# Optimization experiments

Hardware: AMD Instinct MI355X
Metric: run time of the kernel (lower is better)

The kernel has to match this reference:

```python
import jax, jax.numpy as jnp
import numpy as np
from jax import lax

N_NODES = 8192
N_FEAT = 256
N_EDGES = 131072


def _cc_labels(src, dst, n):
    """Weakly-connected-component labels via min-label propagation + pointer jumping.
    Converged label[i] == min node index in i's component (matches scipy's
    first-occurrence labeling order after compaction)."""
    def cond(state):
        return state[1]

    def body(state):
        label, _ = state
        m = jnp.minimum(label[src], label[dst])
        new = label.at[src].min(m).at[dst].min(m)
        new = new[new]  # pointer jump
        return new, jnp.any(new != label)

    label, _ = lax.while_loop(cond, body, (jnp.arange(n, dtype=jnp.int32), jnp.array(True)))
    return label


def setup_inputs() -> dict:
    key = jax.random.key(0)
    k1, k2, k3 = jax.random.split(key, 3)
    x = jax.random.normal(k1, (N_NODES, N_FEAT), dtype=jnp.float32)
    edge_index = jax.random.randint(k2, (2, N_EDGES), 0, N_NODES, dtype=jnp.int32)
    batch = jnp.zeros((N_NODES,), dtype=jnp.int32)
    lin_w = jax.random.normal(k3, (1, 2 * N_FEAT), dtype=jnp.float32) * 0.05
    lin_b = jnp.zeros((1,), dtype=jnp.float32)
    return {"x": x, "edge_index": edge_index, "batch": batch, "lin_w": lin_w, "lin_b": lin_b}


def reference(x, edge_index, batch, lin_w, lin_b):
    n, f = x.shape
    src, dst = edge_index[0], edge_index[1]
    msk = src != dst  # drop self loops (kept in buffer, zeroed via mask for static shapes)
    # undirected: add flipped edges -> 2E directed edges
    src2 = jnp.concatenate([src, dst])
    dst2 = jnp.concatenate([dst, src])
    m2 = jnp.concatenate([msk, msk])
    mf = m2.astype(x.dtype)

    # edge score: Linear(2F,1) on [x[src] || x[dst]] == x@w1 gathered + x@w2 gathered
    w1, w2 = lin_w[0, :f], lin_w[0, f:]
    p1 = x @ w1  # [N]
    p2 = x @ w2  # [N]
    e = jnp.tanh(p1[src2] + p2[dst2] + lin_b[0])  # [2E]

    # contracted edges: score > threshold (0.0); masked edges excluded
    contract = m2 & (e > 0.0)
    srcc = jnp.where(contract, src2, 0)
    dstc = jnp.where(contract, dst2, 0)
    label = _cc_labels(srcc, dstc, n)
    # compact labels in order of smallest node index per component (== scipy ordering)
    is_root = (label == jnp.arange(n, dtype=label.dtype))
    cluster = (jnp.cumsum(is_root.astype(jnp.int32)) - 1)[label]  # [N], values in [0, K)

    # dense adjacency A and score adjacency S (scatter-add, like to_dense_adj)
    A = jnp.zeros((n, n), x.dtype).at[src2, dst2].add(mf)
    S = jnp.zeros((n, n), x.dtype).at[src2, dst2].add(e * mf)

    # isolated nodes w.r.t. contracted adjacency -> S[i,i] = 1
    cint = contract.astype(jnp.int32)
    deg = jnp.zeros(n, jnp.int32).at[src2].add(cint) + jnp.zeros(n, jnp.int32).at[dst2].add(cint)
    isolated = deg == 0
    idx = jnp.arange(n)
    S = S.at[idx, idx].set(jnp.where(isolated, jnp.ones((), x.dtype), S[idx, idx]))

    # X_new = (S @ C).T @ X = C.T @ (S.T @ X)  -- C.T@ is a segment-sum over clusters
    # (padded to N rows; rows >= num_clusters are zero)
    X_new = jax.ops.segment_sum(S.T @ x, cluster, num_segments=n)

    # coarsened adjacency C.T @ A @ C with zero diagonal (dense, padded to NxN)
    M1 = jax.ops.segment_sum(A, cluster, num_segments=n)        # pool rows
    A_c = jax.ops.segment_sum(M1.T, cluster, num_segments=n).T  # pool cols
    A_c = A_c.at[idx, idx].set(0.0)

    new_batch = jnp.zeros(n, batch.dtype).at[cluster].set(batch)
    return X_new, A_c, new_batch, cluster
```

## Files before the change

kernel.cpp:

```cpp
#include <hip/hip_runtime.h>
#include <math.h>

#define N_NODES 8192
#define N_FEAT  256
#define N_EDGES 131072
#define N_DIR   (2*N_EDGES)


__device__ __forceinline__ void edge_sd(const int* __restrict__ ei, int k, int& s, int& d){
  s = ei[k];
  d = (k < N_EDGES) ? ei[k + N_EDGES] : ei[k - N_EDGES];
}

__device__ __forceinline__ int rep_lds(int v, int* L){
  int curr = L[v];
  if (curr != v){
    int prev = v, next;
    while (curr > (next = L[curr])){
      L[prev] = next;
      prev = curr;
      curr = next;
    }
  }
  return curr;
}


__global__ void k_init(int* __restrict__ cnt, int* __restrict__ deg, int* __restrict__ np){
  int i = blockIdx.x * blockDim.x + threadIdx.x;
  if (i < N_NODES){ cnt[i] = 0; deg[i] = 0; }
  if (i == 0) *np = 0;
}

__global__ void k_proj(const float* __restrict__ x, const float* __restrict__ w,
                       float* __restrict__ p1, float* __restrict__ p2){
  int i = blockIdx.x;
  int t = threadIdx.x;
  float v = x[(size_t)i * N_FEAT + t];
  double a = (double)v * (double)w[t];
  double b = (double)v * (double)w[N_FEAT + t];
  for (int off = 32; off; off >>= 1){
    a += __shfl_down(a, off);
    b += __shfl_down(b, off);
  }
  __shared__ double sa[4], sb[4];
  int wid = t >> 6, lane = t & 63;
  if (lane == 0){ sa[wid] = a; sb[wid] = b; }
  __syncthreads();
  if (t == 0){
    p1[i] = (float)(sa[0] + sa[1] + sa[2] + sa[3]);
    p2[i] = (float)(sb[0] + sb[1] + sb[2] + sb[3]);
  }
}

__global__ void k_edges(const int* __restrict__ ei, const float* __restrict__ p1,
                        const float* __restrict__ p2, const float* __restrict__ lb,
                        float* __restrict__ e_val, int* __restrict__ cnt,
                        int* __restrict__ deg, unsigned int* __restrict__ pairs,
                        int* __restrict__ np){
  int k = blockIdx.x * blockDim.x + threadIdx.x;
  int s, d; edge_sd(ei, k, s, d);
  bool selfe = (s == d);
  float e = 0.0f;
  if (!selfe){
    float z = p1[s] + p2[d] + lb[0];
    e = tanhf(z);
    e_val[k] = e;
    atomicAdd(&cnt[d], 1);
    if (e > 0.0f){
      atomicAdd(&deg[s], 1);
      atomicAdd(&deg[d], 1);
    }
  }
  bool c = (!selfe) && (e > 0.0f);
  unsigned long long m = __ballot(c);
  if (m){
    int lane = threadIdx.x & 63;
    int leader = __ffsll((unsigned long long)m) - 1;
    int base = 0;
    if (lane == leader) base = atomicAdd(np, __popcll(m));
    base = __shfl(base, leader);
    if (c){
      int prefix = __popcll(m & ((1ull << lane) - 1ull));
      pairs[base + prefix] = ((unsigned int)s << 13) | (unsigned int)d;
    }
  }
}

__global__ void k_scan(const int* __restrict__ cnt, int* __restrict__ row_start,
                       int* __restrict__ cursor){
  __shared__ int wsum[1024];
  int t = threadIdx.x;
  int base = t * 8;
  int f[8]; int s = 0;
  #pragma unroll
  for (int j = 0; j < 8; ++j){ f[j] = cnt[base + j]; s += f[j]; }
  wsum[t] = s;
  __syncthreads();
  for (int off = 1; off < 1024; off <<= 1){
    int v = (t >= off) ? wsum[t - off] : 0;
    __syncthreads();
    wsum[t] += v;
    __syncthreads();
  }
  int run = wsum[t] - s;
  #pragma unroll
  for (int j = 0; j < 8; ++j){
    row_start[base + j] = run;
    cursor[base + j]    = run;
    run += f[j];
  }
  if (t == 1023) row_start[N_NODES] = run;
}

__global__ void k_fill(const int* __restrict__ ei, const float* __restrict__ e_val,
                       int* __restrict__ cursor, int* __restrict__ esrc, float* __restrict__ evs){
  int k = blockIdx.x * blockDim.x + threadIdx.x;
  if (k >= N_DIR) return;
  int s, d; edge_sd(ei, k, s, d);
  if (s == d) return;
  int slot = atomicAdd(&cursor[d], 1);
  esrc[slot] = s;
  evs[slot]  = e_val[k];
}

__global__ void __launch_bounds__(1024) k_fused(
    const unsigned int* __restrict__ pairs, const int* __restrict__ np,
    const int* __restrict__ batch,
    int* __restrict__ cluster_i, float* __restrict__ out_cluster,
    float* __restrict__ out_batch,
    uint4* __restrict__ zbase, long long n4){
  int t = threadIdx.x;

  if (blockIdx.x != 0){
    long long i = (long long)(blockIdx.x - 1) * blockDim.x + t;
    long long stride = (long long)(gridDim.x - 1) * blockDim.x;
    uint4 z = {0u, 0u, 0u, 0u};
    for (; i < n4; i += stride) zbase[i] = z;
    return;
  }

  __shared__ int L[N_NODES];
  __shared__ int wsum[1024];

  for (int i = t; i < N_NODES; i += 1024) L[i] = i;
  for (int i = t; i < N_NODES; i += 1024) out_batch[i] = 0.0f;
  __syncthreads();

  int n = *np;
  const int CH = 16384;
  for (int cbase = 0; cbase < n; cbase += CH){
    int lim = (cbase + CH < n) ? (cbase + CH) : n;
    for (int k = cbase + t; k < lim; k += 1024){
      unsigned int p = pairs[k];
      int s = (int)(p >> 13), d = (int)(p & 8191u);
      int a = L[s], b = L[d];
      if (a == b) continue;
      a = rep_lds(s, L);
      b = rep_lds(d, L);
      bool repeat;
      do {
        repeat = false;
        if (a != b){
          int ret;
          if (a < b){
            if ((ret = atomicCAS(&L[b], b, a)) != b){ b = ret; repeat = true; }
          } else {
            if ((ret = atomicCAS(&L[a], a, b)) != a){ a = ret; repeat = true; }
          }
        }
      } while (repeat);
    }
    __syncthreads();
    for (int i = t; i < N_NODES; i += 1024){
      int l = L[i];
      while (true){ int q = L[l]; if (q == l) break; l = q; }
      L[i] = l;
    }
    __syncthreads();
  }

  int base = t * 8;
  int l_reg[8];
  #pragma unroll
  for (int j = 0; j < 8; ++j) l_reg[j] = L[base + j];
  __syncthreads();

  int f[8]; int s = 0;
  #pragma unroll
  for (int j = 0; j < 8; ++j){ f[j] = (l_reg[j] == base + j) ? 1 : 0; s += f[j]; }
  wsum[t] = s;
  __syncthreads();
  for (int off = 1; off < 1024; off <<= 1){
    int v = (t >= off) ? wsum[t - off] : 0;
    __syncthreads();
    wsum[t] += v;
    __syncthreads();
  }
  int run = wsum[t] - s;
  #pragma unroll
  for (int j = 0; j < 8; ++j){
    run += f[j];
    if (f[j]) L[base + j] = run - 1;
  }
  __syncthreads();

  #pragma unroll
  for (int j = 0; j < 8; ++j){
    int i = base + j;
    int c = L[l_reg[j]];
    cluster_i[i] = c;
    out_cluster[i] = (float)c;
    out_batch[c] = (float)batch[i];
  }
}

__global__ void k_y(const float* __restrict__ x, const float* __restrict__ evs,
                    const int* __restrict__ esrc, const int* __restrict__ row_start,
                    const int* __restrict__ deg, float* __restrict__ y){
  int i = blockIdx.x;
  int t = threadIdx.x;
  int a = row_start[i], b = row_start[i + 1];
  float acc = (deg[i] == 0) ? x[(size_t)i * N_FEAT + t] : 0.0f;
  for (int j = a; j < b; ++j){
    acc += evs[j] * x[(size_t)esrc[j] * N_FEAT + t];
  }
  y[(size_t)i * N_FEAT + t] = acc;
}

__global__ void k_xnew(const float* __restrict__ y, const int* __restrict__ cluster_i,
                       float* __restrict__ Xn){
  int t = threadIdx.x;
  int node0 = blockIdx.x * 32;
  float acc = 0.0f;
  int cur = cluster_i[node0];
  for (int j = 0; j < 32; ++j){
    int node = node0 + j;
    int c = cluster_i[node];
    if (c != cur){
      atomicAdd(&Xn[(size_t)cur * N_FEAT + t], acc);
      acc = 0.0f; cur = c;
    }
    acc += y[(size_t)node * N_FEAT + t];
  }
  atomicAdd(&Xn[(size_t)cur * N_FEAT + t], acc);
}

__global__ void k_ac(const int* __restrict__ ei, const int* __restrict__ cluster_i,
                     float* __restrict__ Ac){
  int k = blockIdx.x * blockDim.x + threadIdx.x;
  if (k >= N_DIR) return;
  int s, d; edge_sd(ei, k, s, d);
  if (s == d) return;
  int cs = cluster_i[s], cd = cluster_i[d];
  if (cs != cd) atomicAdd(&Ac[(size_t)cs * N_NODES + cd], 1.0f);
}


extern "C" void kernel_launch(void* const* d_in, const int* in_sizes, int n_in,
                              void* d_out, int out_size, void* d_ws, size_t ws_size,
                              hipStream_t stream){
  const float* x     = (const float*)d_in[0];
  const int*   ei    = (const int*)  d_in[1];
  const int*   batch = (const int*)  d_in[2];
  const float* lw    = (const float*)d_in[3];
  const float* lb    = (const float*)d_in[4];

  float* out = (float*)d_out;
  float* Xn  = out;
  float* Ac  = Xn + (size_t)N_NODES * N_FEAT;
  float* ob  = Ac + (size_t)N_NODES * N_NODES;
  float* oc  = ob + N_NODES;

  char* w = (char*)d_ws;
  float* p1        = (float*)w; w += (size_t)N_NODES * 4;
  float* p2        = (float*)w; w += (size_t)N_NODES * 4;
  float* e_val     = (float*)w; w += (size_t)N_DIR   * 4;
  int*   cnt       = (int*)  w; w += (size_t)N_NODES * 4;
  int*   cursor    = (int*)  w; w += (size_t)N_NODES * 4;
  int*   row_start = (int*)  w; w += (size_t)(N_NODES + 8) * 4;
  int*   deg       = (int*)  w; w += (size_t)N_NODES * 4;
  int*   cluster_i = (int*)  w; w += (size_t)N_NODES * 4;
  int*   esrc      = (int*)  w; w += (size_t)N_DIR   * 4;
  float* evs       = (float*)w; w += (size_t)N_DIR   * 4;
  unsigned int* pairs = (unsigned int*)w; w += (size_t)N_DIR * 4;
  int*   np        = (int*)  w; w += 64;
  float* y         = (float*)w; w += (size_t)N_NODES * N_FEAT * 4;

  long long n4 = ((long long)N_NODES * N_FEAT + (long long)N_NODES * N_NODES) / 4;

  k_init  <<<(N_NODES + 255) / 256, 256, 0, stream>>>(cnt, deg, np);
  k_proj  <<<N_NODES, 256, 0, stream>>>(x, lw, p1, p2);
  k_edges <<<N_DIR / 256, 256, 0, stream>>>(ei, p1, p2, lb, e_val, cnt, deg, pairs, np);
  k_scan  <<<1, 1024, 0, stream>>>(cnt, row_start, cursor);
  k_fill  <<<N_DIR / 256, 256, 0, stream>>>(ei, e_val, cursor, esrc, evs);
  k_fused <<<1025, 1024, 0, stream>>>(pairs, np, batch, cluster_i, oc, ob,
                                      (uint4*)out, n4);
  k_y     <<<N_NODES, 256, 0, stream>>>(x, evs, esrc, row_start, deg, y);
  k_xnew  <<<N_NODES / 32, 256, 0, stream>>>(y, cluster_i, Xn);
  k_ac    <<<N_DIR / 256, 256, 0, stream>>>(ei, cluster_i, Ac);
}
```

Measured before the change: 254.9 us.

## Replace CAS union-find with iterative atomicMin label propagation; pack edge data

Connected-component labeling in the single-block fused kernel swaps the CAS-based union-find with path compression for repeated rounds of atomicMin label propagation followed by pointer jumping, looping until a shared flag shows no change. Separately, the CSR edge source and score arrays are interleaved into one uint2 array, so the SpMM kernel issues one 8-byte load per edge instead of two. The propagation approach may need several full passes over all contracted pairs on one block, which could cost more than union-find on large components. It also only updates L[s]/L[d], not their roots, so convergence depends on the pointer-jump step.

```diff
diff --git a/kernel.cpp b/kernel.cpp
--- a/kernel.cpp
+++ b/kernel.cpp
@@ -10,19 +10,6 @@
 __device__ __forceinline__ void edge_sd(const int* __restrict__ ei, int k, int& s, int& d){
   s = ei[k];
   d = (k < N_EDGES) ? ei[k + N_EDGES] : ei[k - N_EDGES];
-}
-
-__device__ __forceinline__ int rep_lds(int v, int* L){
-  int curr = L[v];
-  if (curr != v){
-    int prev = v, next;
-    while (curr > (next = L[curr])){
-      L[prev] = next;
-      prev = curr;
-      curr = next;
-    }
-  }
-  return curr;
 }
 
 
@@ -114,14 +101,14 @@
 }
 
 __global__ void k_fill(const int* __restrict__ ei, const float* __restrict__ e_val,
-                       int* __restrict__ cursor, int* __restrict__ esrc, float* __restrict__ evs){
+                       int* __restrict__ cursor, uint2* __restrict__ edata){
   int k = blockIdx.x * blockDim.x + threadIdx.x;
   if (k >= N_DIR) return;
   int s, d; edge_sd(ei, k, s, d);
   if (s == d) return;
   int slot = atomicAdd(&cursor[d], 1);
-  esrc[slot] = s;
-  evs[slot]  = e_val[k];
+  uint2 v; v.x = (unsigned int)s; v.y = __float_as_uint(e_val[k]);
+  edata[slot] = v;
 }
 
 __global__ void __launch_bounds__(1024) k_fused(
@@ -142,41 +129,33 @@
 
   __shared__ int L[N_NODES];
   __shared__ int wsum[1024];
+  __shared__ int flag;
 
   for (int i = t; i < N_NODES; i += 1024) L[i] = i;
   for (int i = t; i < N_NODES; i += 1024) out_batch[i] = 0.0f;
+  if (t == 0) flag = 0;
   __syncthreads();
 
   int n = *np;
-  const int CH = 16384;
-  for (int cbase = 0; cbase < n; cbase += CH){
-    int lim = (cbase + CH < n) ? (cbase + CH) : n;
-    for (int k = cbase + t; k < lim; k += 1024){
+  while (true){
+    for (int k = t; k < n; k += 1024){
       unsigned int p = pairs[k];
       int s = (int)(p >> 13), d = (int)(p & 8191u);
       int a = L[s], b = L[d];
       if (a == b) continue;
-      a = rep_lds(s, L);
-      b = rep_lds(d, L);
-      bool repeat;
-      do {
-        repeat = false;
-        if (a != b){
-          int ret;
-          if (a < b){
-            if ((ret = atomicCAS(&L[b], b, a)) != b){ b = ret; repeat = true; }
-          } else {
-            if ((ret = atomicCAS(&L[a], a, b)) != a){ a = ret; repeat = true; }
-          }
-        }
-      } while (repeat);
-    }
-    __syncthreads();
+      int m = a < b ? a : b;
+      if (a > m){ int old = atomicMin(&L[s], m); if (old > m) flag = 1; }
+      if (b > m){ int old = atomicMin(&L[d], m); if (old > m) flag = 1; }
+    }
+    __syncthreads();
+    if (!flag) break;
     for (int i = t; i < N_NODES; i += 1024){
       int l = L[i];
       while (true){ int q = L[l]; if (q == l) break; l = q; }
       L[i] = l;
     }
+    __syncthreads();
+    if (t == 0) flag = 0;
     __syncthreads();
   }
 
@@ -215,15 +194,16 @@
   }
 }
 
-__global__ void k_y(const float* __restrict__ x, const float* __restrict__ evs,
-                    const int* __restrict__ esrc, const int* __restrict__ row_start,
+__global__ void k_y(const float* __restrict__ x, const uint2* __restrict__ edata,
+                    const int* __restrict__ row_start,
                     const int* __restrict__ deg, float* __restrict__ y){
   int i = blockIdx.x;
   int t = threadIdx.x;
   int a = row_start[i], b = row_start[i + 1];
   float acc = (deg[i] == 0) ? x[(size_t)i * N_FEAT + t] : 0.0f;
   for (int j = a; j < b; ++j){
-    acc += evs[j] * x[(size_t)esrc[j] * N_FEAT + t];
+    uint2 v = edata[j];
+    acc += __uint_as_float(v.y) * x[(size_t)v.x * N_FEAT + t];
   }
   y[(size_t)i * N_FEAT + t] = acc;
 }
@@ -281,8 +261,7 @@
   int*   row_start = (int*)  w; w += (size_t)(N_NODES + 8) * 4;
   int*   deg       = (int*)  w; w += (size_t)N_NODES * 4;
   int*   cluster_i = (int*)  w; w += (size_t)N_NODES * 4;
-  int*   esrc      = (int*)  w; w += (size_t)N_DIR   * 4;
-  float* evs       = (float*)w; w += (size_t)N_DIR   * 4;
+  uint2* edata     = (uint2*)w; w += (size_t)N_DIR   * 8;
   unsigned int* pairs = (unsigned int*)w; w += (size_t)N_DIR * 4;
   int*   np        = (int*)  w; w += 64;
   float* y         = (float*)w; w += (size_t)N_NODES * N_FEAT * 4;
@@ -293,10 +272,10 @@
   k_proj  <<<N_NODES, 256, 0, stream>>>(x, lw, p1, p2);
   k_edges <<<N_DIR / 256, 256, 0, stream>>>(ei, p1, p2, lb, e_val, cnt, deg, pairs, np);
   k_scan  <<<1, 1024, 0, stream>>>(cnt, row_start, cursor);
-  k_fill  <<<N_DIR / 256, 256, 0, stream>>>(ei, e_val, cursor, esrc, evs);
+  k_fill  <<<N_DIR / 256, 256, 0, stream>>>(ei, e_val, cursor, edata);
   k_fused <<<1025, 1024, 0, stream>>>(pairs, np, batch, cluster_i, oc, ob,
                                       (uint4*)out, n4);
-  k_y     <<<N_NODES, 256, 0, stream>>>(x, evs, esrc, row_start, deg, y);
+  k_y     <<<N_NODES, 256, 0, stream>>>(x, edata, row_start, deg, y);
   k_xnew  <<<N_NODES / 32, 256, 0, stream>>>(y, cluster_i, Xn);
   k_ac    <<<N_DIR / 256, 256, 0, stream>>>(ei, cluster_i, Ac);
 }
```

Result: slower. 271.9 us (+6.7%).
